# Kernel optimization log

Hardware: AMD Instinct MI355X
Metric: run time of the kernel (lower is better)

The kernel has to match this reference:

```python
import jax, jax.numpy as jnp
import numpy as np

EPS = 1e-05
NEG = -1000000000.0

def rmsnorm(x):
    var = jnp.mean(x * x, axis=-1, keepdims=True)
    return x * jax.lax.rsqrt(var + EPS)

def apply_rotary(x, cos, sin):
    # x: [B,T,H,D], cos/sin: [T,D]
    d = x.shape[-1]
    x1, x2 = x[..., : d // 2], x[..., d // 2 :]
    half_rot = jnp.concatenate([-x2, x1], axis=-1)
    c = cos[None, :, None, :]
    s = sin[None, :, None, :]
    return x * c + half_rot * s

def setup_inputs() -> dict:
    key = jax.random.key(0)
    ks = jax.random.split(key, 12)
    B, T, C, H = 2, 2048, 1024, 16
    hd = C // H
    std = 0.02
    return {
        "x": jax.random.normal(ks[0], (B, T, C), jnp.float32),
        "x0": jax.random.normal(ks[1], (B, T, C), jnp.float32),
        "lambdaResid": jnp.ones((), jnp.float32),
        "lambdaX0": jnp.ones((), jnp.float32),
        "cos": jax.random.uniform(ks[2], (T, hd), jnp.float32),
        "sin": jax.random.uniform(ks[3], (T, hd), jnp.float32),
        "qWeight": jax.random.normal(ks[4], (C, C), jnp.float32) * std,
        "kWeight": jax.random.normal(ks[5], (C, C), jnp.float32) * std,
        "vWeight": jax.random.normal(ks[6], (C, C), jnp.float32) * std,
        "projWeight": jax.random.normal(ks[7], (C, C), jnp.float32) * std,
        "fcWeight": jax.random.normal(ks[8], (C, 4 * C), jnp.float32) * std,
        "mlpProjWeight": jax.random.normal(ks[9], (4 * C, C), jnp.float32) * std,
    }

def reference(x, x0, lambdaResid, lambdaX0, cos, sin,
              qWeight, kWeight, vWeight, projWeight, fcWeight, mlpProjWeight):
    B, T, C = x.shape
    hd = cos.shape[-1]
    H = C // hd
    scaled = x * lambdaResid + x0 * lambdaX0
    pre = rmsnorm(scaled)
    q = (pre @ qWeight).reshape(B, T, H, hd)
    k = (pre @ kWeight).reshape(B, T, H, hd)
    v = (pre @ vWeight).reshape(B, T, H, hd)
    q = rmsnorm(apply_rotary(q, cos, sin))  # [B,T,H,D]
    k = rmsnorm(apply_rotary(k, cos, sin))
    scores = jnp.einsum('bthd,bshd->bhts', q, k) / jnp.sqrt(jnp.float32(hd))
    mask = jnp.tril(jnp.ones((T, T), bool))
    scores = jnp.where(mask[None, None], scores, NEG)
    probs = jax.nn.softmax(scores, axis=-1)
    attn = jnp.einsum('bhts,bshd->bthd', probs, v).reshape(B, T, C)
    scaled = scaled + attn @ projWeight
    h = rmsnorm(scaled) @ fcWeight
    h = jnp.square(jax.nn.relu(h))
    return scaled + h @ mlpProjWeight
```

## Files before the change

### kernel.cpp

```cpp
#include <hip/hip_runtime.h>
#include <hip/hip_bf16.h>
#include <stdint.h>

typedef _Float16 f16;
typedef __attribute__((ext_vector_type(8))) _Float16 f16x8;
typedef __attribute__((ext_vector_type(4))) _Float16 f16x4;
typedef __attribute__((ext_vector_type(4))) float f32x4;

__device__ __forceinline__ void g2l16(const void* g, void* l) {
  __builtin_amdgcn_global_load_lds(
      (const __attribute__((address_space(1))) uint32_t*)g,
      (__attribute__((address_space(3))) uint32_t*)l, 16, 0, 0);
}

__global__ __launch_bounds__(256)
void wconv_all_kernel(const float* __restrict__ Wq, const float* __restrict__ Wk,
                      const float* __restrict__ Wv, const float* __restrict__ Wp,
                      const float* __restrict__ Wfc, const float* __restrict__ Wmp,
                      f16* __restrict__ Dq, f16* __restrict__ Dk, f16* __restrict__ Dv,
                      f16* __restrict__ Dp, f16* __restrict__ Dfc, f16* __restrict__ Dmp)
{
  __shared__ float tile[32][33];
  int id = blockIdx.x;
  const float* W; f16* Wt; int K, N, local;
  if      (id < 1024) { W = Wq;  Wt = Dq;  K = 1024; N = 1024; local = id; }
  else if (id < 2048) { W = Wk;  Wt = Dk;  K = 1024; N = 1024; local = id - 1024; }
  else if (id < 3072) { W = Wv;  Wt = Dv;  K = 1024; N = 1024; local = id - 2048; }
  else if (id < 4096) { W = Wp;  Wt = Dp;  K = 1024; N = 1024; local = id - 3072; }
  else if (id < 8192) { W = Wfc; Wt = Dfc; K = 1024; N = 4096; local = id - 4096; }
  else                { W = Wmp; Wt = Dmp; K = 4096; N = 1024; local = id - 8192; }
  int ntx = N >> 5;
  int n0 = (local % ntx) * 32, k0 = (local / ntx) * 32;
  int tx = threadIdx.x & 31, ty = threadIdx.x >> 5;
#pragma unroll
  for (int i = 0; i < 4; ++i)
    tile[ty + 8*i][tx] = W[(size_t)(k0 + ty + 8*i) * N + (n0 + tx)];
  __syncthreads();
#pragma unroll
  for (int i = 0; i < 4; ++i)
    Wt[(size_t)(n0 + ty + 8*i) * K + (k0 + tx)] = (f16)tile[tx][ty + 8*i];
}

__global__ __launch_bounds__(256)
void scale_rms_kernel(const float* __restrict__ x, const float* __restrict__ x0,
                      const float* __restrict__ lamR, const float* __restrict__ lamX,
                      float* __restrict__ scaled, f16* __restrict__ pre)
{
  const int C = 1024;
  int row = blockIdx.x, tid = threadIdx.x;
  float lr = lamR[0], lx = lamX[0];
  size_t base = (size_t)row * C;
  float4 xv = ((const float4*)(x + base))[tid];
  float4 zv = ((const float4*)(x0 + base))[tid];
  float4 sv;
  sv.x = xv.x*lr + zv.x*lx;  sv.y = xv.y*lr + zv.y*lx;
  sv.z = xv.z*lr + zv.z*lx;  sv.w = xv.w*lr + zv.w*lx;
  float ss = sv.x*sv.x + sv.y*sv.y + sv.z*sv.z + sv.w*sv.w;
#pragma unroll
  for (int off = 32; off >= 1; off >>= 1) ss += __shfl_xor(ss, off);
  __shared__ float red[4];
  if ((tid & 63) == 0) red[tid >> 6] = ss;
  __syncthreads();
  float tot = red[0] + red[1] + red[2] + red[3];
  float rs = rsqrtf(tot * (1.0f / 1024.0f) + 1e-5f);
  ((float4*)(scaled + base))[tid] = sv;
  f16* p = pre + base + tid * 4;
  p[0] = (f16)(sv.x * rs); p[1] = (f16)(sv.y * rs);
  p[2] = (f16)(sv.z * rs); p[3] = (f16)(sv.w * rs);
}

__global__ __launch_bounds__(256)
void combine_rms_kernel(const float* __restrict__ resid, const f16* __restrict__ p0,
                        const f16* __restrict__ p1, float* __restrict__ scaled2,
                        f16* __restrict__ pre2)
{
  const int C = 1024;
  int row = blockIdx.x, tid = threadIdx.x;
  size_t base = (size_t)row * C;
  float4 rv = ((const float4*)(resid + base))[tid];
  f16x4 av = ((const f16x4*)(p0 + base))[tid];
  f16x4 bv = ((const f16x4*)(p1 + base))[tid];
  float4 sv;
  sv.x = rv.x + (float)av[0] + (float)bv[0];
  sv.y = rv.y + (float)av[1] + (float)bv[1];
  sv.z = rv.z + (float)av[2] + (float)bv[2];
  sv.w = rv.w + (float)av[3] + (float)bv[3];
  float ss = sv.x*sv.x + sv.y*sv.y + sv.z*sv.z + sv.w*sv.w;
#pragma unroll
  for (int off = 32; off >= 1; off >>= 1) ss += __shfl_xor(ss, off);
  __shared__ float red[4];
  if ((tid & 63) == 0) red[tid >> 6] = ss;
  __syncthreads();
  float tot = red[0] + red[1] + red[2] + red[3];
  float rs = rsqrtf(tot * (1.0f / 1024.0f) + 1e-5f);
  ((float4*)(scaled2 + base))[tid] = sv;
  f16* p = pre2 + base + tid * 4;
  p[0] = (f16)(sv.x * rs); p[1] = (f16)(sv.y * rs);
  p[2] = (f16)(sv.z * rs); p[3] = (f16)(sv.w * rs);
}

__global__ __launch_bounds__(256)
void combine_out4_kernel(const float* __restrict__ resid, const f16* __restrict__ parts,
                         size_t pstride, float* __restrict__ out)
{
  size_t i = (size_t)blockIdx.x * 256 + threadIdx.x;
  float4 rv = ((const float4*)resid)[i];
  float4 sv = rv;
#pragma unroll
  for (int z = 0; z < 4; ++z) {
    f16x4 av = ((const f16x4*)(parts + z * pstride))[i];
    sv.x += (float)av[0]; sv.y += (float)av[1];
    sv.z += (float)av[2]; sv.w += (float)av[3];
  }
  ((float4*)out)[i] = sv;
}

__global__ __launch_bounds__(256)
void rope_rms_kernel(f16* __restrict__ Xq, f16* __restrict__ Xk,
                     const float* __restrict__ cs, const float* __restrict__ sn)
{
  const int MH = 4096 * 16;
  int ridx = blockIdx.x * 4 + (threadIdx.x >> 6);
  f16* X = (ridx < MH) ? Xq : Xk;
  if (ridx >= MH) ridx -= MH;
  int lane = threadIdx.x & 63;
  int h = ridx & 15;
  int bt = ridx >> 4;
  int t = bt & 2047;
  size_t base = (size_t)bt * 1024 + h * 64;
  float xv = (float)X[base + lane];
  float other = __shfl_xor(xv, 32);
  float rot = (lane < 32) ? -other : other;
  float c = cs[t * 64 + lane], s = sn[t * 64 + lane];
  float y = xv * c + rot * s;
  float ss = y * y;
#pragma unroll
  for (int off = 32; off >= 1; off >>= 1) ss += __shfl_xor(ss, off);
  float r = rsqrtf(ss * (1.0f / 64.0f) + 1e-5f);
  X[base + lane] = (f16)(y * r);
}

template<int EPI>
__global__ __launch_bounds__(256)
void gemm_kernel(const f16* __restrict__ A, const f16* __restrict__ Bt,
                 void* __restrict__ out, int M, int N, int K, int nb, int zb)
{
  __shared__ __align__(16) f16 smem[4 * 128 * 32];
  const int tid = threadIdx.x;
  const int wave = tid >> 6, lane = tid & 63;
  const int col = lane & 15, quad = lane >> 4;
  const int id = blockIdx.x;
  const int xcd = id & 7, s = id >> 3;
  const int n_i = s % nb;
  const int p = s / nb;
  const int mpx = (M >> 7) >> 3;
  const int zz = p / mpx;
  const int m_i = xcd * mpx + (p % mpx);
  const int m0 = m_i * 128, n0 = n_i * 128;
  const int wm = (wave >> 1) * 64, wn = (wave & 1) * 64;
  const int Ksub = K / zb;
  const int kBeg = zz * Ksub;
  const int nIter = Ksub >> 5;
  f32x4 acc[4][4] = {};

  const size_t rowb = (size_t)K * 2;
  const char* Agp = (const char*)A  + (size_t)m0 * rowb;
  const char* Bgp = (const char*)Bt + (size_t)n0 * rowb;

  const int r_st = (tid >> 2);
  const int cb_st = (tid & 3) << 4;
  const int lb0 = (wave * 64) << 4;
  const int lb1 = (256 + wave * 64) << 4;

#define STAGE(buf, k0)                                                           \
  {                                                                              \
    const size_t koff = (size_t)(k0) * 2;                                        \
    g2l16(Agp + (size_t)r_st * rowb + koff + cb_st,                              \
          (char*)smem + (buf) * 8192 + lb0);                                     \
    g2l16(Agp + (size_t)(r_st + 64) * rowb + koff + cb_st,                       \
          (char*)smem + (buf) * 8192 + lb1);                                     \
    g2l16(Bgp + (size_t)r_st * rowb + koff + cb_st,                              \
          (char*)smem + 16384 + (buf) * 8192 + lb0);                             \
    g2l16(Bgp + (size_t)(r_st + 64) * rowb + koff + cb_st,                       \
          (char*)smem + 16384 + (buf) * 8192 + lb1);                             \
  }

  STAGE(0, kBeg)
  for (int kt = 0; kt < nIter; ++kt) {
    __syncthreads();
    if (kt + 1 < nIter) STAGE((kt + 1) & 1, kBeg + (kt + 1) * 32)
    const f16* As = smem + (kt & 1) * 4096;
    const f16* Bs = smem + 8192 + (kt & 1) * 4096;
    f16x8 af[4], bf[4];
#pragma unroll
    for (int t = 0; t < 4; ++t)
      af[t] = *(const f16x8*)(As + (wm + t*16 + col) * 32 + quad * 8);
#pragma unroll
    for (int t = 0; t < 4; ++t)
      bf[t] = *(const f16x8*)(Bs + (wn + t*16 + col) * 32 + quad * 8);
#pragma unroll
    for (int mt = 0; mt < 4; ++mt)
#pragma unroll
      for (int nt = 0; nt < 4; ++nt)
        acc[mt][nt] = __builtin_amdgcn_mfma_f32_16x16x32_f16(af[mt], bf[nt], acc[mt][nt], 0, 0, 0);
  }
#undef STAGE
  f16* ep = smem + wave * 1024;
  f16* outz = (EPI == 4) ? ((f16*)out + (size_t)zz * M * N) : (f16*)out;
#pragma unroll
  for (int mt = 0; mt < 4; ++mt) {
#pragma unroll
    for (int nt = 0; nt < 4; ++nt) {
#pragma unroll
      for (int r = 0; r < 4; ++r) {
        float v = acc[mt][nt][r];
        if (EPI == 1) { float tv = v > 0.0f ? v : 0.0f; v = tv * tv; }
        ep[(quad * 4 + r) * 64 + ((nt ^ quad) * 16 + col)] = (f16)v;
      }
    }
#pragma unroll
    for (int j = 0; j < 2; ++j) {
      int e = j * 64 + lane;
      int row = e >> 3, rb = e & 7;
      int phys16 = (((rb >> 1) ^ (row >> 2)) << 1) + (rb & 1);
      f16x8 vv = *(const f16x8*)(ep + row * 64 + phys16 * 8);
      int grow = m0 + wm + mt * 16 + row;
      int gcol = n0 + wn + rb * 8;
      *(f16x8*)(outz + (size_t)grow * N + gcol) = vv;
    }
  }
}

__global__ __launch_bounds__(256)
void gemm_qkv_kernel(const f16* __restrict__ A, const f16* __restrict__ Bt,
                     f16* __restrict__ qb, f16* __restrict__ kbuf, f16* __restrict__ vtg)
{
  const int K = 1024, nb = 24;
  __shared__ __align__(16) f16 smem[4 * 128 * 32];
  const int tid = threadIdx.x;
  const int wave = tid >> 6, lane = tid & 63;
  const int col = lane & 15, quad = lane >> 4;
  const int id = blockIdx.x;
  const int xcd = id & 7, s = id >> 3;
  const int n_i = s % nb;
  const int m_i = xcd * 4 + (s / nb);
  const int m0 = m_i * 128, n0 = n_i * 128;
  const int wm = (wave >> 1) * 64, wn = (wave & 1) * 64;
  f32x4 acc[4][4] = {};

  const size_t rowb = (size_t)K * 2;
  const char* Agp = (const char*)A  + (size_t)m0 * rowb;
  const char* Bgp = (const char*)Bt + (size_t)n0 * rowb;

  const int r_st = (tid >> 2);
  const int cb_st = (tid & 3) << 4;
  const int lb0 = (wave * 64) << 4;
  const int lb1 = (256 + wave * 64) << 4;

#define STAGE(buf, k0)                                                           \
  {                                                                              \
    const size_t koff = (size_t)(k0) * 2;                                        \
    g2l16(Agp + (size_t)r_st * rowb + koff + cb_st,                              \
          (char*)smem + (buf) * 8192 + lb0);                                     \
    g2l16(Agp + (size_t)(r_st + 64) * rowb + koff + cb_st,                       \
          (char*)smem + (buf) * 8192 + lb1);                                     \
    g2l16(Bgp + (size_t)r_st * rowb + koff + cb_st,                              \
          (char*)smem + 16384 + (buf) * 8192 + lb0);                             \
    g2l16(Bgp + (size_t)(r_st + 64) * rowb + koff + cb_st,                       \
          (char*)smem + 16384 + (buf) * 8192 + lb1);                             \
  }

  STAGE(0, 0)
  for (int kt = 0; kt < 32; ++kt) {
    __syncthreads();
    if (kt + 1 < 32) STAGE((kt + 1) & 1, (kt + 1) * 32)
    const f16* As = smem + (kt & 1) * 4096;
    const f16* Bs = smem + 8192 + (kt & 1) * 4096;
    f16x8 af[4], bf[4];
#pragma unroll
    for (int t = 0; t < 4; ++t)
      af[t] = *(const f16x8*)(As + (wm + t*16 + col) * 32 + quad * 8);
#pragma unroll
    for (int t = 0; t < 4; ++t)
      bf[t] = *(const f16x8*)(Bs + (wn + t*16 + col) * 32 + quad * 8);
#pragma unroll
    for (int mt = 0; mt < 4; ++mt)
#pragma unroll
      for (int nt = 0; nt < 4; ++nt)
        acc[mt][nt] = __builtin_amdgcn_mfma_f32_16x16x32_f16(af[mt], bf[nt], acc[mt][nt], 0, 0, 0);
  }
#undef STAGE
  const int cw = n0 + wn;
  const int sel = cw >> 10;
  if (sel < 2) {
    f16* dst = (sel == 0) ? qb : kbuf;
    const int cbase = cw & 1023;
    f16* ep = smem + wave * 1024;
#pragma unroll
    for (int mt = 0; mt < 4; ++mt) {
#pragma unroll
      for (int nt = 0; nt < 4; ++nt)
#pragma unroll
        for (int r = 0; r < 4; ++r)
          ep[(quad * 4 + r) * 64 + ((nt ^ quad) * 16 + col)] = (f16)acc[mt][nt][r];
#pragma unroll
      for (int j = 0; j < 2; ++j) {
        int e = j * 64 + lane;
        int row = e >> 3, rb = e & 7;
        int phys16 = (((rb >> 1) ^ (row >> 2)) << 1) + (rb & 1);
        f16x8 vv = *(const f16x8*)(ep + row * 64 + phys16 * 8);
        int grow = m0 + wm + mt * 16 + row;
        *(f16x8*)(dst + (size_t)grow * 1024 + cbase + rb * 8) = vv;
      }
    }
  } else {
#pragma unroll
    for (int mt = 0; mt < 4; ++mt) {
      int t0 = m0 + wm + mt * 16 + quad * 4;
      int b = t0 >> 11, t = t0 & 2047;
#pragma unroll
      for (int nt = 0; nt < 4; ++nt) {
        int dd = (cw & 1023) + nt * 16 + col;
        int hh = dd >> 6, d = dd & 63;
        f16x4 vv;
#pragma unroll
        for (int r = 0; r < 4; ++r) vv[r] = (f16)acc[mt][nt][r];
        *(f16x4*)(vtg + ((size_t)((b * 16 + hh) * 64 + d)) * 2048 + t) = vv;
      }
    }
  }
}

__global__ __launch_bounds__(256)
void attn_kernel(const f16* __restrict__ Q, const f16* __restrict__ Kc,
                 const f16* __restrict__ Vt, f16* __restrict__ O)
{
  const int T = 2048, C = 1024;
  __shared__ __align__(16) f16 Ks[2][64 * 64];
  __shared__ __align__(16) f16 Vs[2][64 * 64];
  __shared__ __align__(16) f16 Ps[4][16 * 64];
  const int tid = threadIdx.x, wave = tid >> 6, lane = tid & 63;
  const int col = lane & 15, quad = lane >> 4;
  const int bh = blockIdx.x, b = bh >> 4, h = bh & 15;
  const int qt = (int)gridDim.y - 1 - (int)blockIdx.y;
  const int q0 = qt * 64;

  const f16* qb = Q  + ((size_t)b * T) * C + h * 64;
  const f16* kb = Kc + ((size_t)b * T) * C + h * 64;
  const f16* vb = Vt + ((size_t)bh * 64) * T;

  f16x8 aq[2];
#pragma unroll
  for (int ks = 0; ks < 2; ++ks)
    aq[ks] = *(const f16x8*)(qb + (size_t)(q0 + wave*16 + col) * C + ks*32 + quad*8);

  f32x4 o_acc[4];
#pragma unroll
  for (int dt = 0; dt < 4; ++dt) o_acc[dt] = (f32x4){0.f,0.f,0.f,0.f};
  float l_part[4] = {0.f, 0.f, 0.f, 0.f};

  const int srow = lane >> 3;
  const int sblk = (lane & 7) ^ srow;

#pragma unroll
  for (int i = 0; i < 2; ++i) {
    int r0 = wave * 16 + 8 * i;
    g2l16(kb + (size_t)(r0 + srow) * C + sblk * 8, (char*)Ks[0] + r0 * 128);
    g2l16(vb + (size_t)(r0 + srow) * T + sblk * 8, (char*)Vs[0] + r0 * 128);
  }

  int cur = 0;
  for (int kt = 0; kt <= qt; ++kt) {
    __syncthreads();

    if (kt < qt) {
      const int ks1 = (kt + 1) * 64;
#pragma unroll
      for (int i = 0; i < 2; ++i) {
        int r0 = wave * 16 + 8 * i;
        g2l16(kb + (size_t)(ks1 + r0 + srow) * C + sblk * 8, (char*)Ks[cur ^ 1] + r0 * 128);
        g2l16(vb + (size_t)(r0 + srow) * T + ks1 + sblk * 8, (char*)Vs[cur ^ 1] + r0 * 128);
      }
    }

    f32x4 s[4];
#pragma unroll
    for (int nt = 0; nt < 4; ++nt) s[nt] = (f32x4){0.f,0.f,0.f,0.f};
#pragma unroll
    for (int ks = 0; ks < 2; ++ks) {
#pragma unroll
      for (int nt = 0; nt < 4; ++nt) {
        int key = nt * 16 + col;
        f16x8 bk = *(const f16x8*)(Ks[cur] + key * 64 + (((ks*4 + quad) ^ (key & 7)) * 8));
        s[nt] = __builtin_amdgcn_mfma_f32_16x16x32_f16(aq[ks], bk, s[nt], 0, 0, 0);
      }
    }

    const bool masked = (kt == qt);
#pragma unroll
    for (int r = 0; r < 4; ++r) {
      const int qloc = quad * 4 + r;
      float p[4];
#pragma unroll
      for (int nt = 0; nt < 4; ++nt) {
        float pv = __expf(s[nt][r] * 0.125f);
        if (masked && (nt * 16 + col > wave * 16 + qloc)) pv = 0.0f;
        p[nt] = pv;
      }
      l_part[r] += (p[0] + p[1]) + (p[2] + p[3]);
#pragma unroll
      for (int nt = 0; nt < 4; ++nt) {
        int kblk = nt * 2 + (col >> 3);
        Ps[wave][qloc * 64 + ((kblk ^ (qloc & 7)) * 8) + (col & 7)] = (f16)p[nt];
      }
    }

#pragma unroll
    for (int ks = 0; ks < 2; ++ks) {
      f16x8 ap = *(const f16x8*)(&Ps[wave][0] + col * 64 + (((ks*4 + quad) ^ (col & 7)) * 8));
#pragma unroll
      for (int dt = 0; dt < 4; ++dt) {
        int d = dt * 16 + col;
        f16x8 bv = *(const f16x8*)(Vs[cur] + d * 64 + (((ks*4 + quad) ^ (d & 7)) * 8));
        o_acc[dt] = __builtin_amdgcn_mfma_f32_16x16x32_f16(ap, bv, o_acc[dt], 0, 0, 0);
      }
    }
    cur ^= 1;
  }

#pragma unroll
  for (int r = 0; r < 4; ++r) {
#pragma unroll
    for (int off = 8; off >= 1; off >>= 1)
      l_part[r] += __shfl_xor(l_part[r], off, 16);
  }
#pragma unroll
  for (int dt = 0; dt < 4; ++dt) {
#pragma unroll
    for (int r = 0; r < 4; ++r) {
      int qr = q0 + wave * 16 + quad * 4 + r;
      float v = o_acc[dt][r] / l_part[r];
      O[((size_t)b * T + qr) * C + h * 64 + dt * 16 + col] = (f16)v;
    }
  }
}

extern "C" void kernel_launch(void* const* d_in, const int* in_sizes, int n_in,
                              void* d_out, int out_size, void* d_ws, size_t ws_size,
                              hipStream_t stream)
{
  const float* x    = (const float*)d_in[0];
  const float* x0   = (const float*)d_in[1];
  const float* lamR = (const float*)d_in[2];
  const float* lamX = (const float*)d_in[3];
  const float* cs   = (const float*)d_in[4];
  const float* sn   = (const float*)d_in[5];
  const float* Wq   = (const float*)d_in[6];
  const float* Wk   = (const float*)d_in[7];
  const float* Wv   = (const float*)d_in[8];
  const float* Wp   = (const float*)d_in[9];
  const float* Wfc  = (const float*)d_in[10];
  const float* Wmp  = (const float*)d_in[11];
  float* out = (float*)d_out;

  const int B = 2, T = 2048, C = 1024, H = 16;
  const int M = B * T;
  const size_t MB = 1ull << 20;
  char* ws = (char*)d_ws;
  f16*   Wqkv_t = (f16*)(ws + 0 * MB);
  f16*   Wp_t   = (f16*)(ws + 6 * MB);
  f16*   Wfc_t  = (f16*)(ws + 8 * MB);
  f16*   Wmp_t  = (f16*)(ws + 16 * MB);
  float* scaled  = (float*)(ws + 24 * MB);
  f16*   pre     = (f16*)(ws + 40 * MB);
  f16*   qb      = (f16*)(ws + 48 * MB);
  f16*   kbuf    = (f16*)(ws + 56 * MB);
  f16*   vtg     = (f16*)(ws + 64 * MB);
  float* scaled2 = (float*)(ws + 72 * MB);
  f16*   hbuf    = (f16*)(ws + 88 * MB);
  f16*   attnOut = pre;
  f16*   pre2    = qb;
  f16*   projP   = (f16*)(ws + 88 * MB);
  f16*   mlpP    = (f16*)(ws + 24 * MB);

  dim3 tb(256);
  wconv_all_kernel<<<dim3(12288), tb, 0, stream>>>(
      Wq, Wk, Wv, Wp, Wfc, Wmp,
      Wqkv_t, Wqkv_t + 1024*1024, Wqkv_t + 2048*1024, Wp_t, Wfc_t, Wmp_t);

  scale_rms_kernel<<<M, tb, 0, stream>>>(x, x0, lamR, lamX, scaled, pre);

  gemm_qkv_kernel<<<dim3(24 * 32), tb, 0, stream>>>(pre, Wqkv_t, qb, kbuf, vtg);

  rope_rms_kernel<<<(M * H) / 2, tb, 0, stream>>>(qb, kbuf, cs, sn);

  attn_kernel<<<dim3(B * H, T/64), tb, 0, stream>>>(qb, kbuf, vtg, attnOut);

  gemm_kernel<4><<<dim3(8 * 32 * 2), tb, 0, stream>>>(attnOut, Wp_t, projP, M, C, C, 8, 2);
  combine_rms_kernel<<<M, tb, 0, stream>>>(scaled, projP, projP + (size_t)M*C, scaled2, pre2);

  gemm_kernel<1><<<dim3(32 * 32), tb, 0, stream>>>(pre2, Wfc_t, hbuf, M, 4*C, C, 32, 1);

  gemm_kernel<4><<<dim3(8 * 32 * 4), tb, 0, stream>>>(hbuf, Wmp_t, mlpP, M, C, 4*C, 8, 4);
  combine_out4_kernel<<<(M*C)/1024, tb, 0, stream>>>(scaled2, mlpP, (size_t)M*C, out);
}
```

Baseline: 372.8 us.

## Use 256x256 tile GEMMs with 512 threads for QKV and MLP

Replaces the 128x128 QKV GEMM and the MLP fc and down-projection GEMMs with a 256x256 tile, 512-thread kernel. It uses BK=64, XOR-swizzled LDS, double buffering with explicit vmcnt waits, and setprio around the MFMA bursts. Larger tiles raise arithmetic intensity and cut global reloads. In exchange the grids shrink to 192 and 256 blocks on a 256-CU device, so occupancy and the wave-quantization tail may suffer. The down-projection keeps its 4-way split-K so it still has enough blocks.

```diff
diff --git a/kernel.cpp b/kernel.cpp
--- a/kernel.cpp
+++ b/kernel.cpp
@@ -231,65 +231,191 @@
   }
 }
 
-__global__ __launch_bounds__(256)
-void gemm_qkv_kernel(const f16* __restrict__ A, const f16* __restrict__ Bt,
-                     f16* __restrict__ qb, f16* __restrict__ kbuf, f16* __restrict__ vtg)
-{
-  const int K = 1024, nb = 24;
-  __shared__ __align__(16) f16 smem[4 * 128 * 32];
+
+__device__ __forceinline__ void stage256(const char* Agp, const char* Bgp, size_t rowb,
+                                         char* lds, int st_r, size_t koff, int tid)
+{
+#pragma unroll
+  for (int j = 0; j < 4; ++j) {
+    g2l16(Agp + (size_t)(st_r + j * 64) * rowb + koff, lds + j * 8192 + tid * 16);
+    g2l16(Bgp + (size_t)(st_r + j * 64) * rowb + koff, lds + 32768 + j * 8192 + tid * 16);
+  }
+}
+
+template<int EPI>
+__global__ __launch_bounds__(512, 2)
+void gemm256_kernel(const f16* __restrict__ A, const f16* __restrict__ Bt,
+                    void* __restrict__ out, int M, int N, int K, int nb, int zb)
+{
+  __shared__ __align__(16) f16 smem[65536];
   const int tid = threadIdx.x;
   const int wave = tid >> 6, lane = tid & 63;
   const int col = lane & 15, quad = lane >> 4;
   const int id = blockIdx.x;
-  const int xcd = id & 7, s = id >> 3;
-  const int n_i = s % nb;
-  const int m_i = xcd * 4 + (s / nb);
-  const int m0 = m_i * 128, n0 = n_i * 128;
-  const int wm = (wave >> 1) * 64, wn = (wave & 1) * 64;
-  f32x4 acc[4][4] = {};
+  const int xcd = id & 7, sb = id >> 3;
+  const int n_i = sb % nb;
+  const int p = sb / nb;
+  const int mpx = (M >> 8) >> 3;
+  const int zz = p / mpx;
+  const int m_i = xcd * mpx + (p % mpx);
+  const int m0 = m_i * 256, n0 = n_i * 256;
+  const int wm = (wave >> 2) * 128, wn = (wave & 3) * 64;
+  const int Ksub = K / zb;
+  const int kBeg = zz * Ksub;
+  const int ntiles = Ksub >> 6;
+  f32x4 acc[8][4] = {};
 
   const size_t rowb = (size_t)K * 2;
   const char* Agp = (const char*)A  + (size_t)m0 * rowb;
   const char* Bgp = (const char*)Bt + (size_t)n0 * rowb;
 
-  const int r_st = (tid >> 2);
-  const int cb_st = (tid & 3) << 4;
-  const int lb0 = (wave * 64) << 4;
-  const int lb1 = (256 + wave * 64) << 4;
-
-#define STAGE(buf, k0)                                                           \
-  {                                                                              \
-    const size_t koff = (size_t)(k0) * 2;                                        \
-    g2l16(Agp + (size_t)r_st * rowb + koff + cb_st,                              \
-          (char*)smem + (buf) * 8192 + lb0);                                     \
-    g2l16(Agp + (size_t)(r_st + 64) * rowb + koff + cb_st,                       \
-          (char*)smem + (buf) * 8192 + lb1);                                     \
-    g2l16(Bgp + (size_t)r_st * rowb + koff + cb_st,                              \
-          (char*)smem + 16384 + (buf) * 8192 + lb0);                             \
-    g2l16(Bgp + (size_t)(r_st + 64) * rowb + koff + cb_st,                       \
-          (char*)smem + 16384 + (buf) * 8192 + lb1);                             \
-  }
-
-  STAGE(0, 0)
-  for (int kt = 0; kt < 32; ++kt) {
-    __syncthreads();
-    if (kt + 1 < 32) STAGE((kt + 1) & 1, (kt + 1) * 32)
-    const f16* As = smem + (kt & 1) * 4096;
-    const f16* Bs = smem + 8192 + (kt & 1) * 4096;
-    f16x8 af[4], bf[4];
-#pragma unroll
-    for (int t = 0; t < 4; ++t)
-      af[t] = *(const f16x8*)(As + (wm + t*16 + col) * 32 + quad * 8);
-#pragma unroll
-    for (int t = 0; t < 4; ++t)
-      bf[t] = *(const f16x8*)(Bs + (wn + t*16 + col) * 32 + quad * 8);
-#pragma unroll
-    for (int mt = 0; mt < 4; ++mt)
-#pragma unroll
-      for (int nt = 0; nt < 4; ++nt)
-        acc[mt][nt] = __builtin_amdgcn_mfma_f32_16x16x32_f16(af[mt], bf[nt], acc[mt][nt], 0, 0, 0);
-  }
-#undef STAGE
+  const int st_r = tid >> 3;
+  const size_t st_so = (size_t)(((tid & 7) ^ ((tid >> 3) & 7)) << 4);
+
+  stage256(Agp, Bgp, rowb, (char*)smem,         st_r, (size_t)kBeg * 2 + st_so, tid);
+  stage256(Agp, Bgp, rowb, (char*)smem + 65536, st_r, (size_t)(kBeg + 64) * 2 + st_so, tid);
+
+  for (int t = 0; t < ntiles; ++t) {
+    if (t < ntiles - 1) asm volatile("s_waitcnt vmcnt(8)" ::: "memory");
+    else                asm volatile("s_waitcnt vmcnt(0)" ::: "memory");
+    __builtin_amdgcn_s_barrier();
+    asm volatile("" ::: "memory");
+
+    const f16* As = smem + (t & 1) * 32768;
+    const f16* Bs = As + 16384;
+    f16x8 bf[4][2];
+#pragma unroll
+    for (int ct = 0; ct < 4; ++ct)
+#pragma unroll
+      for (int ks = 0; ks < 2; ++ks)
+        bf[ct][ks] = *(const f16x8*)(Bs + (wn + ct*16 + col) * 64 +
+                                     (((ks*4 + quad) ^ (col & 7)) << 3));
+#pragma unroll
+    for (int sp = 0; sp < 4; ++sp) {
+      f16x8 af[2][2];
+#pragma unroll
+      for (int i = 0; i < 2; ++i)
+#pragma unroll
+        for (int ks = 0; ks < 2; ++ks)
+          af[i][ks] = *(const f16x8*)(As + (wm + (sp*2 + i)*16 + col) * 64 +
+                                      (((ks*4 + quad) ^ (col & 7)) << 3));
+      __builtin_amdgcn_s_setprio(1);
+#pragma unroll
+      for (int i = 0; i < 2; ++i)
+#pragma unroll
+        for (int ct = 0; ct < 4; ++ct)
+#pragma unroll
+          for (int ks = 0; ks < 2; ++ks)
+            acc[sp*2 + i][ct] = __builtin_amdgcn_mfma_f32_16x16x32_f16(
+                af[i][ks], bf[ct][ks], acc[sp*2 + i][ct], 0, 0, 0);
+      __builtin_amdgcn_s_setprio(0);
+    }
+
+    asm volatile("s_waitcnt lgkmcnt(0)" ::: "memory");
+    __builtin_amdgcn_s_barrier();
+    asm volatile("" ::: "memory");
+    if (t + 2 < ntiles)
+      stage256(Agp, Bgp, rowb, (char*)smem + (t & 1) * 65536, st_r,
+               (size_t)(kBeg + (t + 2) * 64) * 2 + st_so, tid);
+  }
+
+  f16* ep = smem + wave * 1024;
+  f16* outz = (EPI == 4) ? ((f16*)out + (size_t)zz * M * N) : (f16*)out;
+#pragma unroll
+  for (int mt = 0; mt < 8; ++mt) {
+#pragma unroll
+    for (int ct = 0; ct < 4; ++ct) {
+#pragma unroll
+      for (int r = 0; r < 4; ++r) {
+        float v = acc[mt][ct][r];
+        if (EPI == 1) { float tv = v > 0.0f ? v : 0.0f; v = tv * tv; }
+        ep[(quad * 4 + r) * 64 + ((ct ^ quad) * 16 + col)] = (f16)v;
+      }
+    }
+#pragma unroll
+    for (int j = 0; j < 2; ++j) {
+      int e = j * 64 + lane;
+      int row = e >> 3, rb = e & 7;
+      int phys16 = (((rb >> 1) ^ (row >> 2)) << 1) + (rb & 1);
+      f16x8 vv = *(const f16x8*)(ep + row * 64 + phys16 * 8);
+      int grow = m0 + wm + mt * 16 + row;
+      int gcol = n0 + wn + rb * 8;
+      *(f16x8*)(outz + (size_t)grow * N + gcol) = vv;
+    }
+  }
+}
+
+__global__ __launch_bounds__(512, 2)
+void gemm256_qkv_kernel(const f16* __restrict__ A, const f16* __restrict__ Bt,
+                        f16* __restrict__ qb, f16* __restrict__ kbuf, f16* __restrict__ vtg)
+{
+  const int K = 1024, nb = 12, ntiles = 16;
+  __shared__ __align__(16) f16 smem[65536];
+  const int tid = threadIdx.x;
+  const int wave = tid >> 6, lane = tid & 63;
+  const int col = lane & 15, quad = lane >> 4;
+  const int id = blockIdx.x;
+  const int xcd = id & 7, sb = id >> 3;
+  const int n_i = sb % nb;
+  const int m_i = xcd * 2 + (sb / nb);
+  const int m0 = m_i * 256, n0 = n_i * 256;
+  const int wm = (wave >> 2) * 128, wn = (wave & 3) * 64;
+  f32x4 acc[8][4] = {};
+
+  const size_t rowb = (size_t)K * 2;
+  const char* Agp = (const char*)A  + (size_t)m0 * rowb;
+  const char* Bgp = (const char*)Bt + (size_t)n0 * rowb;
+
+  const int st_r = tid >> 3;
+  const size_t st_so = (size_t)(((tid & 7) ^ ((tid >> 3) & 7)) << 4);
+
+  stage256(Agp, Bgp, rowb, (char*)smem,         st_r, st_so, tid);
+  stage256(Agp, Bgp, rowb, (char*)smem + 65536, st_r, (size_t)64 * 2 + st_so, tid);
+
+  for (int t = 0; t < ntiles; ++t) {
+    if (t < ntiles - 1) asm volatile("s_waitcnt vmcnt(8)" ::: "memory");
+    else                asm volatile("s_waitcnt vmcnt(0)" ::: "memory");
+    __builtin_amdgcn_s_barrier();
+    asm volatile("" ::: "memory");
+
+    const f16* As = smem + (t & 1) * 32768;
+    const f16* Bs = As + 16384;
+    f16x8 bf[4][2];
+#pragma unroll
+    for (int ct = 0; ct < 4; ++ct)
+#pragma unroll
+      for (int ks = 0; ks < 2; ++ks)
+        bf[ct][ks] = *(const f16x8*)(Bs + (wn + ct*16 + col) * 64 +
+                                     (((ks*4 + quad) ^ (col & 7)) << 3));
+#pragma unroll
+    for (int sp = 0; sp < 4; ++sp) {
+      f16x8 af[2][2];
+#pragma unroll
+      for (int i = 0; i < 2; ++i)
+#pragma unroll
+        for (int ks = 0; ks < 2; ++ks)
+          af[i][ks] = *(const f16x8*)(As + (wm + (sp*2 + i)*16 + col) * 64 +
+                                      (((ks*4 + quad) ^ (col & 7)) << 3));
+      __builtin_amdgcn_s_setprio(1);
+#pragma unroll
+      for (int i = 0; i < 2; ++i)
+#pragma unroll
+        for (int ct = 0; ct < 4; ++ct)
+#pragma unroll
+          for (int ks = 0; ks < 2; ++ks)
+            acc[sp*2 + i][ct] = __builtin_amdgcn_mfma_f32_16x16x32_f16(
+                af[i][ks], bf[ct][ks], acc[sp*2 + i][ct], 0, 0, 0);
+      __builtin_amdgcn_s_setprio(0);
+    }
+
+    asm volatile("s_waitcnt lgkmcnt(0)" ::: "memory");
+    __builtin_amdgcn_s_barrier();
+    asm volatile("" ::: "memory");
+    if (t + 2 < ntiles)
+      stage256(Agp, Bgp, rowb, (char*)smem + (t & 1) * 65536, st_r,
+               (size_t)((t + 2) * 64) * 2 + st_so, tid);
+  }
+
   const int cw = n0 + wn;
   const int sel = cw >> 10;
   if (sel < 2) {
@@ -297,12 +423,12 @@
     const int cbase = cw & 1023;
     f16* ep = smem + wave * 1024;
 #pragma unroll
-    for (int mt = 0; mt < 4; ++mt) {
-#pragma unroll
-      for (int nt = 0; nt < 4; ++nt)
+    for (int mt = 0; mt < 8; ++mt) {
+#pragma unroll
+      for (int ct = 0; ct < 4; ++ct)
 #pragma unroll
         for (int r = 0; r < 4; ++r)
-          ep[(quad * 4 + r) * 64 + ((nt ^ quad) * 16 + col)] = (f16)acc[mt][nt][r];
+          ep[(quad * 4 + r) * 64 + ((ct ^ quad) * 16 + col)] = (f16)acc[mt][ct][r];
 #pragma unroll
       for (int j = 0; j < 2; ++j) {
         int e = j * 64 + lane;
@@ -315,16 +441,16 @@
     }
   } else {
 #pragma unroll
-    for (int mt = 0; mt < 4; ++mt) {
+    for (int mt = 0; mt < 8; ++mt) {
       int t0 = m0 + wm + mt * 16 + quad * 4;
       int b = t0 >> 11, t = t0 & 2047;
 #pragma unroll
-      for (int nt = 0; nt < 4; ++nt) {
-        int dd = (cw & 1023) + nt * 16 + col;
+      for (int ct = 0; ct < 4; ++ct) {
+        int dd = (cw & 1023) + ct * 16 + col;
         int hh = dd >> 6, d = dd & 63;
         f16x4 vv;
 #pragma unroll
-        for (int r = 0; r < 4; ++r) vv[r] = (f16)acc[mt][nt][r];
+        for (int r = 0; r < 4; ++r) vv[r] = (f16)acc[mt][ct][r];
         *(f16x4*)(vtg + ((size_t)((b * 16 + hh) * 64 + d)) * 2048 + t) = vv;
       }
     }
@@ -484,13 +610,14 @@
   f16*   mlpP    = (f16*)(ws + 24 * MB);
 
   dim3 tb(256);
+  dim3 tb5(512);
   wconv_all_kernel<<<dim3(12288), tb, 0, stream>>>(
       Wq, Wk, Wv, Wp, Wfc, Wmp,
       Wqkv_t, Wqkv_t + 1024*1024, Wqkv_t + 2048*1024, Wp_t, Wfc_t, Wmp_t);
 
   scale_rms_kernel<<<M, tb, 0, stream>>>(x, x0, lamR, lamX, scaled, pre);
 
-  gemm_qkv_kernel<<<dim3(24 * 32), tb, 0, stream>>>(pre, Wqkv_t, qb, kbuf, vtg);
+  gemm256_qkv_kernel<<<dim3(192), tb5, 0, stream>>>(pre, Wqkv_t, qb, kbuf, vtg);
 
   rope_rms_kernel<<<(M * H) / 2, tb, 0, stream>>>(qb, kbuf, cs, sn);
 
@@ -499,8 +626,8 @@
   gemm_kernel<4><<<dim3(8 * 32 * 2), tb, 0, stream>>>(attnOut, Wp_t, projP, M, C, C, 8, 2);
   combine_rms_kernel<<<M, tb, 0, stream>>>(scaled, projP, projP + (size_t)M*C, scaled2, pre2);
 
-  gemm_kernel<1><<<dim3(32 * 32), tb, 0, stream>>>(pre2, Wfc_t, hbuf, M, 4*C, C, 32, 1);
-
-  gemm_kernel<4><<<dim3(8 * 32 * 4), tb, 0, stream>>>(hbuf, Wmp_t, mlpP, M, C, 4*C, 8, 4);
+  gemm256_kernel<1><<<dim3(256), tb5, 0, stream>>>(pre2, Wfc_t, hbuf, M, 4*C, C, 16, 1);
+
+  gemm256_kernel<4><<<dim3(256), tb5, 0, stream>>>(hbuf, Wmp_t, mlpP, M, C, 4*C, 4, 4);
   combine_out4_kernel<<<(M*C)/1024, tb, 0, stream>>>(scaled2, mlpP, (size_t)M*C, out);
 }
```

After: 349.8 us. -6.2%, faster.
